# Kernel tuning notes

Hardware: AMD Instinct MI355X
Metric: run time of the kernel (lower is better)

Reference implementation:

```python
import jax, jax.numpy as jnp
import numpy as np

N_NODES = 100000
N_EDGES = 3200000
N_GRAPHS = 1000


def transformer_conv(x, src, dst, Wq, bq, Wk, bk, Wv, bv, Ws, bs, num_nodes):
    """PyG TransformerConv, heads=1, concat=True, root_weight=True, beta=False.
    Message flows src -> dst; softmax over incoming edges of each dst node."""
    d = Wq.shape[1]
    q = x @ Wq + bq                                   # [N, d]
    k = x @ Wk + bk                                   # [N, d]
    v = x @ Wv + bv                                   # [N, d]
    s = (q[dst] * k[src]).sum(-1) / jnp.sqrt(jnp.asarray(d, x.dtype))  # [E]
    smax = jax.ops.segment_max(s, dst, num_segments=num_nodes)         # [N]
    smax = jnp.where(jnp.isfinite(smax), smax, 0.0)   # nodes with no in-edges
    e = jnp.exp(s - smax[dst])                        # [E]
    denom = jax.ops.segment_sum(e, dst, num_segments=num_nodes)        # [N]
    alpha = e / jnp.maximum(denom[dst], 1e-16)        # [E]
    agg = jax.ops.segment_sum(alpha[:, None] * v[src], dst, num_segments=num_nodes)
    return agg + x @ Ws + bs                          # skip connection (lin_skip)


def setup_inputs() -> dict:
    key = jax.random.key(0)
    ks = jax.random.split(key, 20)
    x = jax.random.normal(ks[0], (N_NODES, 11), dtype=jnp.float32)
    edge_index = jax.random.randint(ks[1], (2, N_EDGES), 0, N_NODES, dtype=jnp.int64)
    batch = jnp.sort(jax.random.randint(ks[2], (N_NODES,), 0, N_GRAPHS, dtype=jnp.int64))

    def lin(k, fan_in, fan_out):
        kw, kb = jax.random.split(k)
        s = 1.0 / np.sqrt(fan_in)
        W = jax.random.uniform(kw, (fan_in, fan_out), jnp.float32, -s, s)
        b = jax.random.uniform(kb, (fan_out,), jnp.float32, -s, s)
        return W, b

    Wq1, bq1 = lin(ks[3], 11, 16); Wk1, bk1 = lin(ks[4], 11, 16)
    Wv1, bv1 = lin(ks[5], 11, 16); Ws1, bs1 = lin(ks[6], 11, 16)
    Wq2, bq2 = lin(ks[7], 16, 32); Wk2, bk2 = lin(ks[8], 16, 32)
    Wv2, bv2 = lin(ks[9], 16, 32); Ws2, bs2 = lin(ks[10], 16, 32)
    Wf1, bf1 = lin(ks[11], 32, 64)
    Wf2, bf2 = lin(ks[12], 64, 1)
    return dict(x=x, edge_index=edge_index, batch=batch,
                Wq1=Wq1, bq1=bq1, Wk1=Wk1, bk1=bk1, Wv1=Wv1, bv1=bv1, Ws1=Ws1, bs1=bs1,
                Wq2=Wq2, bq2=bq2, Wk2=Wk2, bk2=bk2, Wv2=Wv2, bv2=bv2, Ws2=Ws2, bs2=bs2,
                Wf1=Wf1, bf1=bf1, Wf2=Wf2, bf2=bf2)


def reference(x, edge_index, batch,
              Wq1, bq1, Wk1, bk1, Wv1, bv1, Ws1, bs1,
              Wq2, bq2, Wk2, bk2, Wv2, bv2, Ws2, bs2,
              Wf1, bf1, Wf2, bf2):
    src, dst = edge_index[0], edge_index[1]
    h = jax.nn.relu(transformer_conv(x, src, dst, Wq1, bq1, Wk1, bk1, Wv1, bv1, Ws1, bs1, N_NODES))
    h = jax.nn.relu(transformer_conv(h, src, dst, Wq2, bq2, Wk2, bk2, Wv2, bv2, Ws2, bs2, N_NODES))
    # global_mean_pool over graphs
    sums = jax.ops.segment_sum(h, batch, num_segments=N_GRAPHS)            # [G, 32]
    counts = jax.ops.segment_sum(jnp.ones((h.shape[0],), h.dtype), batch, num_segments=N_GRAPHS)
    g = sums / jnp.maximum(counts, 1.0)[:, None]
    g = jax.nn.relu(g @ Wf1 + bf1)
    return g @ Wf2 + bf2                                                   # [G, 1]
```

## Files before the change

### kernel.cpp

```cpp
#include <hip/hip_runtime.h>
#include <hip/hip_bf16.h>
#include <math.h>

#define N_NODES  100000
#define N_EDGES  3200000
#define N_GRAPHS 1000
#define NBKT ((N_NODES + 255) >> 8)
#define BCAP 9216
#define PCHUNK 4096
#define EPT (PCHUNK / 256)
#define DBIN 128

__device__ __forceinline__ unsigned short f2bf(float f) {
    unsigned u = __float_as_uint(f);
    return (unsigned short)((u + 0x7FFFu + ((u >> 16) & 1u)) >> 16);
}
__device__ __forceinline__ void unpack2(unsigned u, float& a, float& b) {
    a = __uint_as_float(u << 16);
    b = __uint_as_float(u & 0xFFFF0000u);
}

__global__ void detect_kernel(const long long* __restrict__ idx, int* __restrict__ flag) {
    int t = threadIdx.x;
    unsigned long long hi = ((unsigned long long)idx[t]) >> 32;
    unsigned long long any = __ballot(hi != 0ull);
    if (t == 0) *flag = (any == 0ull) ? 1 : 0;
}

__global__ __launch_bounds__(256)
void init_kernel(unsigned* __restrict__ bcur, float* __restrict__ pool,
                 float* __restrict__ cnt) {
    int t = blockIdx.x * blockDim.x + threadIdx.x;
    if (t < NBKT)         bcur[t] = (unsigned)t * BCAP;
    if (t < N_GRAPHS*32)  pool[t] = 0.f;
    if (t < N_GRAPHS)     cnt[t]  = 0.f;
}

__global__ __launch_bounds__(256)
void partition_kernel(const int* __restrict__ idx32, const long long* __restrict__ idx64,
                      const int* __restrict__ flag,
                      unsigned* __restrict__ bcur, unsigned* __restrict__ srtp) {
    __shared__ unsigned       sbuf[PCHUNK];
    __shared__ unsigned short sbkt[PCHUNK];
    __shared__ unsigned lhist[NBKT];
    __shared__ unsigned lscan[512];
    __shared__ unsigned gbase[NBKT];
    const int is64 = *flag;
    const int t = threadIdx.x;
    const int base = blockIdx.x * PCHUNK;
    const int nval = min(PCHUNK, N_EDGES - base);

    for (int b = t; b < NBKT; b += 256) lhist[b] = 0u;
    __syncthreads();

    unsigned pr[EPT]; unsigned short br[EPT]; unsigned short rr[EPT];
    #pragma unroll
    for (int r = 0; r < EPT; ++r) {
        int e = base + r * 256 + t;
        br[r] = 0xFFFF;
        if (e < N_EDGES) {
            int s = is64 ? (int)idx64[e]           : idx32[e];
            int d = is64 ? (int)idx64[N_EDGES + e] : idx32[N_EDGES + e];
            unsigned bk = ((unsigned)d) >> 8;
            pr[r] = (((unsigned)d & 255u) << 17) | (unsigned)s;
            br[r] = (unsigned short)bk;
            rr[r] = (unsigned short)atomicAdd(&lhist[bk], 1u);
        }
    }
    __syncthreads();

    lscan[t]       = (t < NBKT)       ? lhist[t]       : 0u;
    lscan[t + 256] = (t + 256 < NBKT) ? lhist[t + 256] : 0u;
    __syncthreads();
    for (int off = 1; off < 512; off <<= 1) {
        unsigned v0 = (t >= off)       ? lscan[t - off]       : 0u;
        unsigned v1 = (t + 256 >= off) ? lscan[t + 256 - off] : 0u;
        __syncthreads();
        lscan[t] += v0; lscan[t + 256] += v1;
        __syncthreads();
    }

    for (int b = t; b < NBKT; b += 256) {
        unsigned c = lhist[b];
        if (c) gbase[b] = atomicAdd(&bcur[b], c);
    }

    #pragma unroll
    for (int r = 0; r < EPT; ++r) {
        if (br[r] != 0xFFFF) {
            unsigned b = br[r];
            unsigned slot = lscan[b] - lhist[b] + rr[r];
            sbuf[slot] = pr[r];
            sbkt[slot] = (unsigned short)b;
        }
    }
    __syncthreads();

    for (int slot = t; slot < nval; slot += 256) {
        unsigned p = sbuf[slot];
        unsigned b = sbkt[slot];
        unsigned lst = lscan[b] - lhist[b];
        srtp[gbase[b] + ((unsigned)slot - lst)] = p;
    }
}

__global__ __launch_bounds__(256)
void build_kernel(unsigned* __restrict__ srtp, const unsigned* __restrict__ bcur,
                  int* __restrict__ row_start, int* __restrict__ row_end,
                  unsigned* __restrict__ dhb) {
    __shared__ unsigned sbuf[BCAP];
    __shared__ int      sdst[BCAP];
    __shared__ unsigned ldeg[256];
    __shared__ unsigned lsc[256];
    __shared__ int      lcur[256];
    __shared__ unsigned ldh[DBIN];
    const int b = blockIdx.x;
    const int t = threadIdx.x;
    const int segbase = b * BCAP;
    const int cntb = min((int)bcur[b] - segbase, BCAP);

    ldeg[t] = 0u;
    if (t < DBIN) ldh[t] = 0u;
    __syncthreads();
    for (int e = t; e < cntb; e += 256) {
        unsigned p = srtp[segbase + e];
        sbuf[e] = p;
        atomicAdd(&ldeg[p >> 17], 1u);
    }
    __syncthreads();
    lsc[t] = ldeg[t];
    __syncthreads();
    for (int off = 1; off < 256; off <<= 1) {
        unsigned v = (t >= off) ? lsc[t - off] : 0u;
        __syncthreads();
        lsc[t] += v;
        __syncthreads();
    }
    int excl = (int)(lsc[t] - ldeg[t]);
    int node = (b << 8) + t;
    if (node < N_NODES) {
        row_start[node] = segbase + excl;
        row_end[node]   = segbase + excl + (int)ldeg[t];
        atomicAdd(&ldh[min((int)ldeg[t], DBIN - 1)], 1u);
    }
    lcur[t] = excl;
    __syncthreads();
    if (t < DBIN) dhb[(size_t)b * DBIN + t] = ldh[t];
    for (int e = t; e < cntb; e += 256) {
        unsigned p = sbuf[e];
        int pos = atomicAdd(&lcur[p >> 17], 1);
        sdst[pos] = (int)(p & 0x1FFFFu);
    }
    __syncthreads();

    const int wave = t >> 6, lane = t & 63;
    for (int n = wave; n < 256; n += 4) {
        int len = (int)ldeg[n];
        if (len < 2 || len > 64) continue;
        int lofs = (int)(lsc[n] - ldeg[n]);
        int v = (lane < len) ? sdst[lofs + lane] : 0x7FFFFFFF;
        #pragma unroll
        for (int k = 2; k <= 64; k <<= 1) {
            #pragma unroll
            for (int j = k >> 1; j > 0; j >>= 1) {
                int pv = __shfl_xor(v, j, 64);
                bool up    = (lane & k) == 0;
                bool lower = (lane & j) == 0;
                int mn = min(v, pv), mx = max(v, pv);
                v = (up == lower) ? mn : mx;
            }
        }
        if (lane < len) sdst[lofs + lane] = v;
    }
    __syncthreads();
    for (int e = t; e < cntb; e += 256)
        srtp[segbase + e] = (unsigned)sdst[e];
}

__global__ __launch_bounds__(512)
void pscan_kernel(unsigned* __restrict__ dhb, unsigned* __restrict__ dh) {
    __shared__ unsigned s[512];
    const int bin = blockIdx.x;
    const int t = threadIdx.x;
    unsigned v = (t < NBKT) ? dhb[(size_t)t * DBIN + bin] : 0u;
    s[t] = v;
    __syncthreads();
    for (int off = 1; off < 512; off <<= 1) {
        unsigned add = (t >= off) ? s[t - off] : 0u;
        __syncthreads();
        s[t] += add;
        __syncthreads();
    }
    if (t < NBKT) dhb[(size_t)t * DBIN + bin] = s[t] - v;
    if (t == 511) dh[bin] = s[511];
}

__global__ __launch_bounds__(DBIN)
void degscan_kernel(const unsigned* __restrict__ dh, unsigned* __restrict__ dcur) {
    __shared__ unsigned s[DBIN];
    const int t = threadIdx.x;
    unsigned v = dh[DBIN - 1 - t];
    s[t] = v;
    __syncthreads();
    for (int off = 1; off < DBIN; off <<= 1) {
        unsigned add = (t >= off) ? s[t - off] : 0u;
        __syncthreads();
        s[t] += add;
        __syncthreads();
    }
    dcur[DBIN - 1 - t] = s[t] - v;
}

__global__ __launch_bounds__(256)
void degscatter_kernel(const int* __restrict__ row_start, const int* __restrict__ row_end,
                       const unsigned* __restrict__ dcur, const unsigned* __restrict__ dhb,
                       int* __restrict__ perm) {
    __shared__ unsigned lh[DBIN];
    const int t = threadIdx.x;
    const int blk = blockIdx.x;
    const int i = blk * 256 + t;
    if (t < DBIN) lh[t] = 0u;
    __syncthreads();
    if (i < N_NODES) {
        int d = min(row_end[i] - row_start[i], DBIN - 1);
        unsigned rank = atomicAdd(&lh[d], 1u);
        perm[dcur[d] + dhb[(size_t)blk * DBIN + d] + rank] = i;
    }
}

template <int IN, int OUT>
__global__ __launch_bounds__(256)
void lin_kernel(const float* __restrict__ x,
                const float* __restrict__ Wq, const float* __restrict__ bq,
                const float* __restrict__ Wk, const float* __restrict__ bk,
                const float* __restrict__ Wv, const float* __restrict__ bv,
                const float* __restrict__ Ws, const float* __restrict__ bs,
                float scale,
                float* __restrict__ q, unsigned short* __restrict__ kv,
                float* __restrict__ sk, int n)
{
    __shared__ float w[4 * IN * OUT];
    __shared__ float b[4 * OUT];
    for (int t = threadIdx.x; t < IN * OUT; t += blockDim.x) {
        w[t]            = Wq[t];
        w[IN*OUT + t]   = Wk[t];
        w[2*IN*OUT + t] = Wv[t];
        w[3*IN*OUT + t] = Ws[t];
    }
    for (int t = threadIdx.x; t < OUT; t += blockDim.x) {
        b[t]         = bq[t];
        b[OUT + t]   = bk[t];
        b[2*OUT + t] = bv[t];
        b[3*OUT + t] = bs[t];
    }
    __syncthreads();

    for (int i = blockIdx.x * blockDim.x + threadIdx.x; i < n;
         i += gridDim.x * blockDim.x) {
        float xi[IN];
        #pragma unroll
        for (int r = 0; r < IN; ++r) xi[r] = x[(size_t)i * IN + r];

        #pragma unroll
        for (int j = 0; j < OUT; ++j) {
            float aq = b[j], ak = b[OUT + j], av = b[2*OUT + j], as = b[3*OUT + j];
            #pragma unroll
            for (int r = 0; r < IN; ++r) {
                float xr = xi[r];
                aq += xr * w[r*OUT + j];
                ak += xr * w[IN*OUT + r*OUT + j];
                av += xr * w[2*IN*OUT + r*OUT + j];
                as += xr * w[3*IN*OUT + r*OUT + j];
            }
            int c = j >> 2, r4 = j & 3;
            q[(size_t)i * OUT + j]                  = aq * scale;
            kv[(size_t)i * 2 * OUT + c * 8 + r4]     = f2bf(ak);
            kv[(size_t)i * 2 * OUT + c * 8 + 4 + r4] = f2bf(av);
            sk[(size_t)i * OUT + j]                 = as;
        }
    }
}

template <int D, bool POOL>
__global__ __launch_bounds__(256)
void fused_attn_kernel(const float* __restrict__ q, const unsigned short* __restrict__ kv,
                       const float* __restrict__ sk,
                       const int* __restrict__ row_start, const int* __restrict__ row_end,
                       const unsigned* __restrict__ sorted_src,
                       const int* __restrict__ perm,
                       const int* __restrict__ b32, const long long* __restrict__ b64,
                       const int* __restrict__ flag,
                       float* __restrict__ h, float* __restrict__ pool,
                       float* __restrict__ cnt)
{
    constexpr int L = D / 4;
    const int gpb = 256 / L;
    const int lj = threadIdx.x & (L - 1);
    int g = blockIdx.x * gpb + threadIdx.x / L;
    if (g >= N_NODES) return;
    const int i = perm[g];

    const float4 qj = *(const float4*)(q + (size_t)i * D + lj * 4);
    const int beg = row_start[i], end = row_end[i];

    float m = -INFINITY, denom = 0.f;
    float4 acc = make_float4(0.f, 0.f, 0.f, 0.f);

    if (beg < end) {
        const int last = end - 1;

        int s0 = (int)sorted_src[min(beg + 0, last)];
        int s1 = (int)sorted_src[min(beg + 1, last)];
        int s2 = (int)sorted_src[min(beg + 2, last)];
        int s3 = (int)sorted_src[min(beg + 3, last)];
        uint4 A0 = ((const uint4*)(kv + (size_t)s0 * (2 * D)))[lj];
        uint4 A1 = ((const uint4*)(kv + (size_t)s1 * (2 * D)))[lj];
        uint4 B0 = ((const uint4*)(kv + (size_t)s2 * (2 * D)))[lj];
        uint4 B1 = ((const uint4*)(kv + (size_t)s3 * (2 * D)))[lj];

        for (int e = beg; e < end; e += 4) {
            {
                int sn0 = (int)sorted_src[min(e + 4, last)];
                int sn1 = (int)sorted_src[min(e + 5, last)];
                float k0,k1,k2,k3, l0,l1,l2,l3;
                unpack2(A0.x, k0, k1); unpack2(A0.y, k2, k3);
                unpack2(A1.x, l0, l1); unpack2(A1.y, l2, l3);
                float pa = k0*qj.x + k1*qj.y + k2*qj.z + k3*qj.w;
                float pb = l0*qj.x + l1*qj.y + l2*qj.z + l3*qj.w;
                #pragma unroll
                for (int off = L / 2; off; off >>= 1) {
                    pa += __shfl_xor(pa, off, L);
                    pb += __shfl_xor(pb, off, L);
                }
                if (e + 1 > last) pb = -INFINITY;
                float mn = fmaxf(m, fmaxf(pa, pb));
                float so = __expf(m - mn);
                float w0 = __expf(pa - mn);
                float w1 = __expf(pb - mn);
                float u0,u1,u2,u3, t0,t1,t2,t3;
                unpack2(A0.z, u0, u1); unpack2(A0.w, u2, u3);
                unpack2(A1.z, t0, t1); unpack2(A1.w, t2, t3);
                denom = denom * so + w0 + w1;
                acc.x = acc.x * so + w0 * u0 + w1 * t0;
                acc.y = acc.y * so + w0 * u1 + w1 * t1;
                acc.z = acc.z * so + w0 * u2 + w1 * t2;
                acc.w = acc.w * so + w0 * u3 + w1 * t3;
                m = mn;
                A0 = ((const uint4*)(kv + (size_t)sn0 * (2 * D)))[lj];
                A1 = ((const uint4*)(kv + (size_t)sn1 * (2 * D)))[lj];
            }
            {
                int sn0 = (int)sorted_src[min(e + 6, last)];
                int sn1 = (int)sorted_src[min(e + 7, last)];
                float k0,k1,k2,k3, l0,l1,l2,l3;
                unpack2(B0.x, k0, k1); unpack2(B0.y, k2, k3);
                unpack2(B1.x, l0, l1); unpack2(B1.y, l2, l3);
                float pa = k0*qj.x + k1*qj.y + k2*qj.z + k3*qj.w;
                float pb = l0*qj.x + l1*qj.y + l2*qj.z + l3*qj.w;
                #pragma unroll
                for (int off = L / 2; off; off >>= 1) {
                    pa += __shfl_xor(pa, off, L);
                    pb += __shfl_xor(pb, off, L);
                }
                if (e + 2 > last) pa = -INFINITY;
                if (e + 3 > last) pb = -INFINITY;
                float mn = fmaxf(m, fmaxf(pa, pb));
                float so = __expf(m - mn);
                float w0 = __expf(pa - mn);
                float w1 = __expf(pb - mn);
                float u0,u1,u2,u3, t0,t1,t2,t3;
                unpack2(B0.z, u0, u1); unpack2(B0.w, u2, u3);
                unpack2(B1.z, t0, t1); unpack2(B1.w, t2, t3);
                denom = denom * so + w0 + w1;
                acc.x = acc.x * so + w0 * u0 + w1 * t0;
                acc.y = acc.y * so + w0 * u1 + w1 * t1;
                acc.z = acc.z * so + w0 * u2 + w1 * t2;
                acc.w = acc.w * so + w0 * u3 + w1 * t3;
                m = mn;
                B0 = ((const uint4*)(kv + (size_t)sn0 * (2 * D)))[lj];
                B1 = ((const uint4*)(kv + (size_t)sn1 * (2 * D)))[lj];
            }
        }
    }

    float dn = 1.f / fmaxf(denom, 1e-16f);
    const float4 skv = *(const float4*)(sk + (size_t)i * D + lj * 4);
    float4 o;
    o.x = fmaxf(acc.x * dn + skv.x, 0.f);
    o.y = fmaxf(acc.y * dn + skv.y, 0.f);
    o.z = fmaxf(acc.z * dn + skv.z, 0.f);
    o.w = fmaxf(acc.w * dn + skv.w, 0.f);

    if (POOL) {
        int b = (*flag) ? (int)b64[i] : b32[i];
        float* pb = pool + b * 32 + lj * 4;
        atomicAdd(pb + 0, o.x);
        atomicAdd(pb + 1, o.y);
        atomicAdd(pb + 2, o.z);
        atomicAdd(pb + 3, o.w);
        if (lj == 0) atomicAdd(&cnt[b], 1.f);
    } else {
        *(float4*)(h + (size_t)i * D + lj * 4) = o;
    }
}

__global__ __launch_bounds__(64)
void mlp_kernel(const float* __restrict__ pool, const float* __restrict__ cnt,
                const float* __restrict__ Wf1, const float* __restrict__ bf1,
                const float* __restrict__ Wf2, const float* __restrict__ bf2,
                float* __restrict__ out)
{
    int g = blockIdx.x;
    int h = threadIdx.x;
    __shared__ float m[32];
    if (h < 32) {
        float c = fmaxf(cnt[g], 1.f);
        m[h] = pool[g * 32 + h] / c;
    }
    __syncthreads();
    float acc = bf1[h];
    #pragma unroll
    for (int r = 0; r < 32; ++r) acc += m[r] * Wf1[r * 64 + h];
    float hid = fmaxf(acc, 0.f);
    float c = hid * Wf2[h];
    #pragma unroll
    for (int off = 32; off; off >>= 1) c += __shfl_xor(c, off, 64);
    if (h == 0) out[g] = c + bf2[0];
}

extern "C" void kernel_launch(void* const* d_in, const int* in_sizes, int n_in,
                              void* d_out, int out_size, void* d_ws, size_t ws_size,
                              hipStream_t stream) {
    const float* x = (const float*)d_in[0];
    const void*  edge_index = d_in[1];
    const void*  batch      = d_in[2];
    const float* Wq1 = (const float*)d_in[3];  const float* bq1 = (const float*)d_in[4];
    const float* Wk1 = (const float*)d_in[5];  const float* bk1 = (const float*)d_in[6];
    const float* Wv1 = (const float*)d_in[7];  const float* bv1 = (const float*)d_in[8];
    const float* Ws1 = (const float*)d_in[9];  const float* bs1 = (const float*)d_in[10];
    const float* Wq2 = (const float*)d_in[11]; const float* bq2 = (const float*)d_in[12];
    const float* Wk2 = (const float*)d_in[13]; const float* bk2 = (const float*)d_in[14];
    const float* Wv2 = (const float*)d_in[15]; const float* bv2 = (const float*)d_in[16];
    const float* Ws2 = (const float*)d_in[17]; const float* bs2 = (const float*)d_in[18];
    const float* Wf1 = (const float*)d_in[19]; const float* bf1 = (const float*)d_in[20];
    const float* Wf2 = (const float*)d_in[21]; const float* bf2 = (const float*)d_in[22];
    float* out = (float*)d_out;

    char* ws = (char*)d_ws;
    size_t off = 0;
    auto carve = [&](size_t bytes) {
        char* p = ws + off;
        off = (off + bytes + 255) & ~(size_t)255;
        return p;
    };
    int*            flag     = (int*)            carve(16);
    int*            row_start= (int*)            carve((size_t)N_NODES * 4);
    int*            row_end  = (int*)            carve((size_t)N_NODES * 4);
    unsigned*       bcur     = (unsigned*)       carve((size_t)NBKT * 4);
    float*          pool     = (float*)          carve((size_t)N_GRAPHS * 32 * 4);
    float*          cnt      = (float*)          carve((size_t)N_GRAPHS * 4);
    unsigned*       dh       = (unsigned*)       carve((size_t)DBIN * 4);
    unsigned*       dcur     = (unsigned*)       carve((size_t)DBIN * 4);
    unsigned*       dhb      = (unsigned*)       carve((size_t)NBKT * DBIN * 4);
    int*            perm     = (int*)            carve((size_t)N_NODES * 4);
    unsigned*       srtp     = (unsigned*)       carve((size_t)NBKT * BCAP * 4);
    float*          qb       = (float*)          carve((size_t)N_NODES * 32 * 4);
    unsigned short* kvb      = (unsigned short*) carve((size_t)N_NODES * 64 * 2);
    float*          skb      = (float*)          carve((size_t)N_NODES * 32 * 4);
    float*          h1       = (float*)          carve((size_t)N_NODES * 16 * 4);
    (void)ws_size; (void)in_sizes; (void)n_in; (void)out_size;

    const int* ei32 = (const int*)edge_index;
    const long long* ei64 = (const long long*)edge_index;
    const int* b32 = (const int*)batch;
    const long long* b64 = (const long long*)batch;

    const dim3 blk(256);

    detect_kernel<<<1, 64, 0, stream>>>(ei64, flag);
    init_kernel<<<(N_GRAPHS * 32 + 255) / 256, blk, 0, stream>>>(bcur, pool, cnt);
    partition_kernel<<<(N_EDGES + PCHUNK - 1) / PCHUNK, blk, 0, stream>>>(
        ei32, ei64, flag, bcur, srtp);
    build_kernel<<<NBKT, blk, 0, stream>>>(srtp, bcur, row_start, row_end, dhb);
    pscan_kernel<<<DBIN, 512, 0, stream>>>(dhb, dh);
    degscan_kernel<<<1, DBIN, 0, stream>>>(dh, dcur);
    degscatter_kernel<<<NBKT, blk, 0, stream>>>(row_start, row_end, dcur, dhb, perm);

    lin_kernel<11, 16><<<(N_NODES + 255) / 256, blk, 0, stream>>>(
        x, Wq1, bq1, Wk1, bk1, Wv1, bv1, Ws1, bs1, 0.25f,
        qb, kvb, skb, N_NODES);
    fused_attn_kernel<16, false><<<(N_NODES + 63) / 64, blk, 0, stream>>>(
        qb, kvb, skb, row_start, row_end, srtp, perm, b32, b64, flag, h1, pool, cnt);

    lin_kernel<16, 32><<<(N_NODES + 255) / 256, blk, 0, stream>>>(
        h1, Wq2, bq2, Wk2, bk2, Wv2, bv2, Ws2, bs2, 0.17677669529663688f,
        qb, kvb, skb, N_NODES);
    fused_attn_kernel<32, true><<<(N_NODES + 31) / 32, blk, 0, stream>>>(
        qb, kvb, skb, row_start, row_end, srtp, perm, b32, b64, flag, nullptr, pool, cnt);

    mlp_kernel<<<N_GRAPHS, 64, 0, stream>>>(pool, cnt, Wf1, bf1, Wf2, bf2, out);
}
```

Before: 347.9 us.

## Fold dtype detect into init, vectorize edge loads, drop build LDS staging

Merges the index-width detection into the init kernel, removing one launch. The partition kernel now loads two edges per thread with 128-bit (int64) or 64-bit (int32) vector loads instead of scalar loads, which changes which edges each thread handles. The build kernel drops its shared-memory copy of the bucket and reads it from global memory twice, freeing about 36 KB of LDS per block for occupancy at the cost of a second global read, which is likely cache-resident.

```diff
diff --git a/kernel.cpp b/kernel.cpp
--- a/kernel.cpp
+++ b/kernel.cpp
@@ -20,17 +20,16 @@
     b = __uint_as_float(u & 0xFFFF0000u);
 }
 
-__global__ void detect_kernel(const long long* __restrict__ idx, int* __restrict__ flag) {
-    int t = threadIdx.x;
-    unsigned long long hi = ((unsigned long long)idx[t]) >> 32;
-    unsigned long long any = __ballot(hi != 0ull);
-    if (t == 0) *flag = (any == 0ull) ? 1 : 0;
-}
-
 __global__ __launch_bounds__(256)
-void init_kernel(unsigned* __restrict__ bcur, float* __restrict__ pool,
+void init_kernel(const long long* __restrict__ idx, int* __restrict__ flag,
+                 unsigned* __restrict__ bcur, float* __restrict__ pool,
                  float* __restrict__ cnt) {
     int t = blockIdx.x * blockDim.x + threadIdx.x;
+    if (blockIdx.x == 0 && threadIdx.x < 64) {
+        unsigned long long hi = ((unsigned long long)idx[threadIdx.x]) >> 32;
+        unsigned long long any = __ballot(hi != 0ull);
+        if (threadIdx.x == 0) *flag = (any == 0ull) ? 1 : 0;
+    }
     if (t < NBKT)         bcur[t] = (unsigned)t * BCAP;
     if (t < N_GRAPHS*32)  pool[t] = 0.f;
     if (t < N_GRAPHS)     cnt[t]  = 0.f;
@@ -55,16 +54,27 @@
 
     unsigned pr[EPT]; unsigned short br[EPT]; unsigned short rr[EPT];
     #pragma unroll
-    for (int r = 0; r < EPT; ++r) {
-        int e = base + r * 256 + t;
-        br[r] = 0xFFFF;
-        if (e < N_EDGES) {
-            int s = is64 ? (int)idx64[e]           : idx32[e];
-            int d = is64 ? (int)idx64[N_EDGES + e] : idx32[N_EDGES + e];
-            unsigned bk = ((unsigned)d) >> 8;
-            pr[r] = (((unsigned)d & 255u) << 17) | (unsigned)s;
-            br[r] = (unsigned short)bk;
-            rr[r] = (unsigned short)atomicAdd(&lhist[bk], 1u);
+    for (int r = 0; r < EPT / 2; ++r) {
+        int e0 = base + r * 512 + 2 * t;
+        br[2*r] = 0xFFFF; br[2*r+1] = 0xFFFF;
+        if (e0 < N_EDGES) {
+            int s0, s1, d0, d1;
+            if (is64) {
+                longlong2 sp = *(const longlong2*)(idx64 + e0);
+                longlong2 dp = *(const longlong2*)(idx64 + N_EDGES + e0);
+                s0 = (int)sp.x; s1 = (int)sp.y; d0 = (int)dp.x; d1 = (int)dp.y;
+            } else {
+                int2 sp = *(const int2*)(idx32 + e0);
+                int2 dp = *(const int2*)(idx32 + N_EDGES + e0);
+                s0 = sp.x; s1 = sp.y; d0 = dp.x; d1 = dp.y;
+            }
+            unsigned bk0 = ((unsigned)d0) >> 8, bk1 = ((unsigned)d1) >> 8;
+            pr[2*r]   = (((unsigned)d0 & 255u) << 17) | (unsigned)s0;
+            pr[2*r+1] = (((unsigned)d1 & 255u) << 17) | (unsigned)s1;
+            br[2*r]   = (unsigned short)bk0;
+            br[2*r+1] = (unsigned short)bk1;
+            rr[2*r]   = (unsigned short)atomicAdd(&lhist[bk0], 1u);
+            rr[2*r+1] = (unsigned short)atomicAdd(&lhist[bk1], 1u);
         }
     }
     __syncthreads();
@@ -108,7 +118,6 @@
 void build_kernel(unsigned* __restrict__ srtp, const unsigned* __restrict__ bcur,
                   int* __restrict__ row_start, int* __restrict__ row_end,
                   unsigned* __restrict__ dhb) {
-    __shared__ unsigned sbuf[BCAP];
     __shared__ int      sdst[BCAP];
     __shared__ unsigned ldeg[256];
     __shared__ unsigned lsc[256];
@@ -122,11 +131,8 @@
     ldeg[t] = 0u;
     if (t < DBIN) ldh[t] = 0u;
     __syncthreads();
-    for (int e = t; e < cntb; e += 256) {
-        unsigned p = srtp[segbase + e];
-        sbuf[e] = p;
-        atomicAdd(&ldeg[p >> 17], 1u);
-    }
+    for (int e = t; e < cntb; e += 256)
+        atomicAdd(&ldeg[srtp[segbase + e] >> 17], 1u);
     __syncthreads();
     lsc[t] = ldeg[t];
     __syncthreads();
@@ -147,7 +153,7 @@
     __syncthreads();
     if (t < DBIN) dhb[(size_t)b * DBIN + t] = ldh[t];
     for (int e = t; e < cntb; e += 256) {
-        unsigned p = sbuf[e];
+        unsigned p = srtp[segbase + e];
         int pos = atomicAdd(&lcur[p >> 17], 1);
         sdst[pos] = (int)(p & 0x1FFFFu);
     }
@@ -477,8 +483,7 @@
 
     const dim3 blk(256);
 
-    detect_kernel<<<1, 64, 0, stream>>>(ei64, flag);
-    init_kernel<<<(N_GRAPHS * 32 + 255) / 256, blk, 0, stream>>>(bcur, pool, cnt);
+    init_kernel<<<(N_GRAPHS * 32 + 255) / 256, blk, 0, stream>>>(ei64, flag, bcur, pool, cnt);
     partition_kernel<<<(N_EDGES + PCHUNK - 1) / PCHUNK, blk, 0, stream>>>(
         ei32, ei64, flag, bcur, srtp);
     build_kernel<<<NBKT, blk, 0, stream>>>(srtp, bcur, row_start, row_end, dhb);
```

New measurement: 343.7 us. About the same (-1.2%).
